# Kernel optimization log

Hardware: AMD Instinct MI355X
Metric: run time of the kernel (lower is better)

## Reference

```python
import jax, jax.numpy as jnp
import numpy as np

T, HID, HQ, HKV, D = 2048, 4096, 32, 8, 128
ROPE_BASE = 10000.0


def setup_inputs() -> dict:
    key = jax.random.key(0)
    ks = jax.random.split(key, 5)
    scale = 0.02
    hidden_states = jax.random.normal(ks[0], (T, HID), dtype=jnp.float32)
    position_ids = jnp.arange(T, dtype=jnp.int32)
    # HF-style rotary tables: freqs duplicated along last dim -> [T, D]
    inv_freq = 1.0 / (ROPE_BASE ** (jnp.arange(0, D, 2, dtype=jnp.float32) / D))
    ang = position_ids.astype(jnp.float32)[:, None] * inv_freq[None, :]  # [T, D/2]
    emb = jnp.concatenate([ang, ang], axis=-1)  # [T, D]
    cos, sin = jnp.cos(emb), jnp.sin(emb)
    Wq = jax.random.normal(ks[1], (HID, HQ * D), dtype=jnp.float32) * scale
    Wk = jax.random.normal(ks[2], (HID, HKV * D), dtype=jnp.float32) * scale
    Wv = jax.random.normal(ks[3], (HID, HKV * D), dtype=jnp.float32) * scale
    Wo = jax.random.normal(ks[4], (HQ * D, HID), dtype=jnp.float32) * scale
    return {"hidden_states": hidden_states, "position_ids": position_ids,
            "cos": cos, "sin": sin, "Wq": Wq, "Wk": Wk, "Wv": Wv, "Wo": Wo}


def _rotate_half(x):
    x1, x2 = jnp.split(x, 2, axis=-1)
    return jnp.concatenate([-x2, x1], axis=-1)


def reference(hidden_states, position_ids, cos, sin, Wq, Wk, Wv, Wo):
    t = hidden_states.shape[0]
    scaling = D ** -0.5
    # QKV projections (attention_bias=False)
    q = (hidden_states @ Wq).reshape(t, HQ, D)   # [T, Hq, D]
    k = (hidden_states @ Wk).reshape(t, HKV, D)  # [T, Hkv, D]
    v = (hidden_states @ Wv).reshape(t, HKV, D)
    # RoPE: cos/sin [T, D] broadcast over heads
    c, s = cos[:, None, :], sin[:, None, :]
    q = q * c + _rotate_half(q) * s
    k = k * c + _rotate_half(k) * s
    # GQA: expand KV heads to query heads
    groups = HQ // HKV
    k = jnp.repeat(k, groups, axis=1)  # [T, Hq, D]
    v = jnp.repeat(v, groups, axis=1)
    # Causal attention
    scores = jnp.einsum('thd,shd->hts', q, k) * scaling  # [Hq, T, T]
    causal = jnp.tril(jnp.ones((t, t), dtype=bool))
    scores = jnp.where(causal[None], scores, jnp.finfo(scores.dtype).min)
    probs = jax.nn.softmax(scores, axis=-1)
    attn = jnp.einsum('hts,shd->thd', probs, v).reshape(t, HQ * D)
    return attn @ Wo
```

## Files before the change

kernel.cpp:

```cpp
#include <hip/hip_runtime.h>
#include <hip/hip_bf16.h>
#include <cstdint>
#include <cstddef>

#define T_DIM   2048
#define HID     4096
#define HQ      32
#define HKV     8
#define D_HEAD  128
#define QKV_N   6144
#define KOFF    4096
#define VOFF    5120

typedef __attribute__((ext_vector_type(8))) short short8;
typedef __attribute__((ext_vector_type(4))) float floatx4;

__device__ __forceinline__ ushort f2bf(float f) {
    union { float f; uint u; } v; v.f = f;
    uint r = v.u + 0x7fffu + ((v.u >> 16) & 1u);
    return (ushort)(r >> 16);
}
__device__ __forceinline__ float bf2f(ushort h) {
    union { uint u; float f; } v; v.u = ((uint)h) << 16; return v.f;
}
__device__ __forceinline__ short8 ld8(const ushort* p) {
    uint2 a = *(const uint2*)p, b = *(const uint2*)(p + 4);
    union { uint u[4]; short8 s; } x;
    x.u[0] = a.x; x.u[1] = a.y; x.u[2] = b.x; x.u[3] = b.y;
    return x.s;
}
__device__ __forceinline__ void gld_lds16(const ushort* g, ushort* l) {
    __builtin_amdgcn_global_load_lds(
        (__attribute__((address_space(1))) void*)(g),
        (__attribute__((address_space(3))) void*)(l), 16, 0, 0);
}

__global__ void cast_f32_bf16(const float* __restrict__ in, ushort* __restrict__ out, int n) {
    int i = (blockIdx.x * blockDim.x + threadIdx.x) * 4;
    if (i < n) {
        float4 v = *(const float4*)(in + i);
        ushort4 o;
        o.x = f2bf(v.x); o.y = f2bf(v.y); o.z = f2bf(v.z); o.w = f2bf(v.w);
        *(ushort4*)(out + i) = o;
    }
}

__global__ __launch_bounds__(256) void transpose_cast(const float* __restrict__ W,
                                                      ushort* __restrict__ Wt, int K, int N) {
    __shared__ ushort tile[64][66];
    int n0 = blockIdx.x * 64, k0 = blockIdx.y * 64;
    int tx = threadIdx.x & 15, ty = threadIdx.x >> 4;
#pragma unroll
    for (int i = 0; i < 4; i++) {
        int r = ty + i * 16;
        float4 v = *(const float4*)&W[(size_t)(k0 + r) * N + n0 + tx * 4];
        tile[tx * 4 + 0][r] = f2bf(v.x);
        tile[tx * 4 + 1][r] = f2bf(v.y);
        tile[tx * 4 + 2][r] = f2bf(v.z);
        tile[tx * 4 + 3][r] = f2bf(v.w);
    }
    __syncthreads();
#pragma unroll
    for (int i = 0; i < 4; i++) {
        int nr = ty + i * 16;
        ushort4 o = *(const ushort4*)&tile[nr][tx * 4];
        *(ushort4*)&Wt[(size_t)(n0 + nr) * K + k0 + tx * 4] = o;
    }
}

__global__ void transpose_v(const ushort* __restrict__ qkv, ushort* __restrict__ VtG) {
    __shared__ ushort tile[32][33];
    int t0 = blockIdx.x * 32, d0 = blockIdx.y * 32, kvh = blockIdx.z;
    int tx = threadIdx.x & 31, ty = threadIdx.x >> 5;
#pragma unroll
    for (int i = 0; i < 4; i++) {
        int t = t0 + ty + i * 8;
        tile[ty + i * 8][tx] = qkv[(size_t)t * QKV_N + VOFF + kvh * D_HEAD + d0 + tx];
    }
    __syncthreads();
#pragma unroll
    for (int i = 0; i < 4; i++) {
        int d = d0 + ty + i * 8;
        VtG[((size_t)kvh * D_HEAD + d) * T_DIM + t0 + tx] = tile[tx][ty + i * 8];
    }
}

template <typename OutT>
__global__ __launch_bounds__(256) void gemm_bt(const ushort* __restrict__ A,
                                               const ushort* __restrict__ Bt,
                                               OutT* __restrict__ C,
                                               int K, int lda, int ldb, int ldc) {
    __shared__ ushort As[2][128 * 32];
    __shared__ ushort Bs[2][128 * 32];
    int tid = threadIdx.x;
    int w = tid >> 6, lane = tid & 63, quad = lane >> 4, l15 = lane & 15;
    int wr = (w >> 1) * 64, wc = (w & 1) * 64;
    int m0 = blockIdx.x * 128, n0 = blockIdx.y * 128;

    floatx4 acc[4][4];
    floatx4 z = {0.f, 0.f, 0.f, 0.f};
#pragma unroll
    for (int i = 0; i < 4; i++)
#pragma unroll
        for (int j = 0; j < 4; j++) acc[i][j] = z;

    int arow = tid >> 2, ac = (tid & 3) * 8;
    const ushort* gA0 = A + (size_t)(m0 + arow) * lda + ac;
    const ushort* gA1 = A + (size_t)(m0 + arow + 64) * lda + ac;
    const ushort* gB0 = Bt + (size_t)(n0 + arow) * ldb + ac;
    const ushort* gB1 = Bt + (size_t)(n0 + arow + 64) * ldb + ac;

    gld_lds16(gA0, &As[0][tid * 8]);
    gld_lds16(gA1, &As[0][64 * 32 + tid * 8]);
    gld_lds16(gB0, &Bs[0][tid * 8]);
    gld_lds16(gB1, &Bs[0][64 * 32 + tid * 8]);
    gA0 += 32; gA1 += 32; gB0 += 32; gB1 += 32;

    int cur = 0;
    for (int k0 = 0; k0 < K; k0 += 32, cur ^= 1) {
        __syncthreads();
        if (k0 + 32 < K) {
            gld_lds16(gA0, &As[cur ^ 1][tid * 8]);
            gld_lds16(gA1, &As[cur ^ 1][64 * 32 + tid * 8]);
            gld_lds16(gB0, &Bs[cur ^ 1][tid * 8]);
            gld_lds16(gB1, &Bs[cur ^ 1][64 * 32 + tid * 8]);
            gA0 += 32; gA1 += 32; gB0 += 32; gB1 += 32;
        }

        short8 af[4];
#pragma unroll
        for (int i = 0; i < 4; i++)
            af[i] = *(const short8*)&As[cur][(wr + i * 16 + l15) * 32 + quad * 8];
#pragma unroll
        for (int j = 0; j < 4; j++) {
            short8 bf = *(const short8*)&Bs[cur][(wc + j * 16 + l15) * 32 + quad * 8];
#pragma unroll
            for (int i = 0; i < 4; i++)
                acc[i][j] = __builtin_amdgcn_mfma_f32_16x16x32_bf16(af[i], bf, acc[i][j], 0, 0, 0);
        }
    }

#pragma unroll
    for (int i = 0; i < 4; i++) {
        int row0 = m0 + wr + i * 16 + quad * 4;
#pragma unroll
        for (int j = 0; j < 4; j++) {
            int col = n0 + wc + j * 16 + l15;
#pragma unroll
            for (int r = 0; r < 4; r++) {
                float v = acc[i][j][r];
                if constexpr (sizeof(OutT) == 2)
                    C[(size_t)(row0 + r) * ldc + col] = (OutT)f2bf(v);
                else
                    C[(size_t)(row0 + r) * ldc + col] = v;
            }
        }
    }
}

__global__ void rope_kernel(ushort* __restrict__ qkv, const float* __restrict__ cosb,
                            const float* __restrict__ sinb) {
    int t = blockIdx.x;
    ushort* row = qkv + (size_t)t * QKV_N;
    const float* cr = cosb + (size_t)t * D_HEAD;
    const float* sr = sinb + (size_t)t * D_HEAD;
    for (int c = threadIdx.x; c < 2560; c += 256) {
        int slice = c >> 6, d = c & 63;
        int col = slice * 128 + d;
        float x0 = bf2f(row[col]), x1 = bf2f(row[col + 64]);
        float cs = cr[d], sn = sr[d];
        row[col] = f2bf(x0 * cs - x1 * sn);
        row[col + 64] = f2bf(x1 * cs + x0 * sn);
    }
}

#define PS_STRIDE 68

__global__ __launch_bounds__(256, 2) void attn_kernel(const ushort* __restrict__ qkv,
                                                      const ushort* __restrict__ VtG,
                                                      ushort* __restrict__ attn) {
    __shared__ ushort Ks[64 * 128];
    __shared__ ushort Vt[128 * 64];
    __shared__ ushort Ps[128 * PS_STRIDE];

    int qt = (gridDim.x - 1) - blockIdx.x;
    int h = blockIdx.y;
    int q0 = qt * 128;
    int kbmax = 2 * qt + 1;
    int tid = threadIdx.x, w = tid >> 6, lane = tid & 63, quad = lane >> 4, l15 = lane & 15;
    int kvh = h >> 2;

    const ushort* kbase = qkv + (size_t)KOFF + (size_t)kvh * D_HEAD;
    const ushort* vbase = VtG + (size_t)kvh * D_HEAD * T_DIM;

    const ushort* ksrc[4];
    const ushort* vsrc[4];
#pragma unroll
    for (int i = 0; i < 4; i++) {
        int cid = i * 256 + tid;
        int kr = cid >> 4, kp = cid & 15, kc = kp ^ (kr & 15);
        ksrc[i] = kbase + (size_t)kr * QKV_N + kc * 8;
        int vr = cid >> 3, vp = cid & 7, vc = vp ^ (vr & 7);
        vsrc[i] = vbase + (size_t)vr * T_DIM + vc * 8;
    }

#pragma unroll
    for (int i = 0; i < 4; i++) {
        gld_lds16(ksrc[i], &Ks[(i * 256 + tid) * 8]);
        ksrc[i] += (size_t)64 * QKV_N;
    }

    short8 qf[2][4];
#pragma unroll
    for (int s = 0; s < 2; s++) {
        const ushort* qrow = qkv + (size_t)(q0 + s * 64 + w * 16 + l15) * QKV_N + h * D_HEAD + quad * 8;
#pragma unroll
        for (int ks = 0; ks < 4; ks++)
            qf[s][ks] = *(const short8*)(qrow + ks * 32);
    }

    floatx4 o[2][8];
    floatx4 z = {0.f, 0.f, 0.f, 0.f};
#pragma unroll
    for (int s = 0; s < 2; s++)
#pragma unroll
        for (int j = 0; j < 8; j++) o[s][j] = z;
    float lsum[2][4] = {{0.f, 0.f, 0.f, 0.f}, {0.f, 0.f, 0.f, 0.f}};

    const float scale_l2e = 0.08838834764831845f * 1.4426950408889634f;
    const float BOUND = 24.0f;

    __syncthreads();

    for (int kb = 0; kb <= kbmax; kb++) {
        bool act0 = (kb <= 2 * qt);

#pragma unroll
        for (int i = 0; i < 4; i++) {
            gld_lds16(vsrc[i], &Vt[(i * 256 + tid) * 8]);
            vsrc[i] += 64;
        }

        floatx4 sc[2][4];
#pragma unroll
        for (int s = 0; s < 2; s++)
#pragma unroll
            for (int jt = 0; jt < 4; jt++) sc[s][jt] = z;
#pragma unroll
        for (int ks = 0; ks < 4; ks++) {
#pragma unroll
            for (int jt = 0; jt < 4; jt++) {
                short8 kf = ld8(&Ks[(jt * 16 + l15) * 128 + (((ks * 4 + quad) ^ l15) * 8)]);
                if (act0)
                    sc[0][jt] = __builtin_amdgcn_mfma_f32_16x16x32_bf16(qf[0][ks], kf, sc[0][jt], 0, 0, 0);
                sc[1][jt] = __builtin_amdgcn_mfma_f32_16x16x32_bf16(qf[1][ks], kf, sc[1][jt], 0, 0, 0);
            }
        }

#pragma unroll
        for (int s = 0; s < 2; s++) {
            if (s == 0 && !act0) continue;
            bool diag = (kb == 2 * qt + s);
#pragma unroll
            for (int r = 0; r < 4; r++) {
                int rloc = w * 16 + quad * 4 + r;
#pragma unroll
                for (int jt = 0; jt < 4; jt++) {
                    float v = fmaf(sc[s][jt][r], scale_l2e, -BOUND);
                    if (diag && (jt * 16 + l15 > rloc)) v = -1e30f;
                    float p = exp2f(v);
                    lsum[s][r] += p;
                    Ps[(s * 64 + rloc) * PS_STRIDE + jt * 16 + l15] = f2bf(p);
                }
            }
        }

        __syncthreads();

        if (kb < kbmax) {
#pragma unroll
            for (int i = 0; i < 4; i++) {
                gld_lds16(ksrc[i], &Ks[(i * 256 + tid) * 8]);
                ksrc[i] += (size_t)64 * QKV_N;
            }
        }

#pragma unroll
        for (int ks2 = 0; ks2 < 2; ks2++) {
            short8 pf0 = ld8(&Ps[(w * 16 + l15) * PS_STRIDE + ks2 * 32 + quad * 8]);
            short8 pf1 = ld8(&Ps[(64 + w * 16 + l15) * PS_STRIDE + ks2 * 32 + quad * 8]);
#pragma unroll
            for (int jt = 0; jt < 8; jt++) {
                short8 vf = ld8(&Vt[(jt * 16 + l15) * 64 + (((ks2 * 4 + quad) ^ (l15 & 7)) * 8)]);
                if (act0)
                    o[0][jt] = __builtin_amdgcn_mfma_f32_16x16x32_bf16(pf0, vf, o[0][jt], 0, 0, 0);
                o[1][jt] = __builtin_amdgcn_mfma_f32_16x16x32_bf16(pf1, vf, o[1][jt], 0, 0, 0);
            }
        }

        __syncthreads();
    }

#pragma unroll
    for (int s = 0; s < 2; s++) {
#pragma unroll
        for (int r = 0; r < 4; r++) {
            float l = lsum[s][r];
#pragma unroll
            for (int mk = 1; mk <= 8; mk <<= 1) l += __shfl_xor(l, mk);
            float inv = 1.f / l;
            int trow = q0 + s * 64 + w * 16 + quad * 4 + r;
            ushort* orow = attn + (size_t)trow * (HQ * D_HEAD) + h * D_HEAD;
#pragma unroll
            for (int jt = 0; jt < 8; jt++)
                orow[jt * 16 + l15] = f2bf(o[s][jt][r] * inv);
        }
    }
}

extern "C" void kernel_launch(void* const* d_in, const int* in_sizes, int n_in,
                              void* d_out, int out_size, void* d_ws, size_t ws_size,
                              hipStream_t stream) {
    const float* hidden = (const float*)d_in[0];
    const float* cosb = (const float*)d_in[2];
    const float* sinb = (const float*)d_in[3];
    const float* Wq = (const float*)d_in[4];
    const float* Wk = (const float*)d_in[5];
    const float* Wv = (const float*)d_in[6];
    const float* Wo = (const float*)d_in[7];
    float* out = (float*)d_out;

    char* ws = (char*)d_ws;
    ushort* hiddenB = (ushort*)(ws);
    ushort* WqkvT   = (ushort*)(ws + (size_t)(16u << 20));
    ushort* WoT     = (ushort*)(ws + (size_t)(64u << 20));
    ushort* qkv     = (ushort*)(ws + (size_t)(96u << 20));
    ushort* attnO   = (ushort*)(ws + (size_t)(120u << 20));
    ushort* VtG     = (ushort*)(ws + (size_t)(136u << 20));

    cast_f32_bf16<<<8192, 256, 0, stream>>>(hidden, hiddenB, T_DIM * HID);
    transpose_cast<<<dim3(64, 64), 256, 0, stream>>>(Wq, WqkvT, HID, 4096);
    transpose_cast<<<dim3(16, 64), 256, 0, stream>>>(Wk, WqkvT + (size_t)4096 * HID, HID, 1024);
    transpose_cast<<<dim3(16, 64), 256, 0, stream>>>(Wv, WqkvT + (size_t)5120 * HID, HID, 1024);
    transpose_cast<<<dim3(64, 64), 256, 0, stream>>>(Wo, WoT, HID, 4096);

    gemm_bt<ushort><<<dim3(16, 48), 256, 0, stream>>>(hiddenB, WqkvT, qkv,
                                                      HID, HID, HID, QKV_N);
    rope_kernel<<<T_DIM, 256, 0, stream>>>(qkv, cosb, sinb);
    transpose_v<<<dim3(64, 4, 8), 256, 0, stream>>>(qkv, VtG);
    attn_kernel<<<dim3(T_DIM / 128, HQ), 256, 0, stream>>>(qkv, VtG, attnO);
    gemm_bt<float><<<dim3(16, 32), 256, 0, stream>>>(attnO, WoT, out,
                                                     HID, HID, HID, HID);
}
```

Measured before the change: 542.4 us.

## Replace GEMM with 256x256-tile, 4-stage pipelined, swizzled-LDS 8-wave kernel

Swaps the 128x128 double-buffered GEMM for a 256x256 tile kernel with 512 threads, a 4-deep LDS ring buffer with prefetch three steps ahead, XOR-swizzled LDS layout to avoid bank conflicts, and explicit waitcnt/barrier/setprio scheduling to overlap loads with MFMA. The goal is more data reuse per tile and better hiding of global-load latency in both projection GEMMs. In exchange, LDS use is large (128KB) and the grid is small (192 and 128 blocks), which may underfill the CUs. The manual vmcnt bookkeeping also risks subtle hazards.

```diff
diff --git a/kernel.cpp b/kernel.cpp
--- a/kernel.cpp
+++ b/kernel.cpp
@@ -86,68 +86,107 @@
 }
 
 template <typename OutT>
-__global__ __launch_bounds__(256) void gemm_bt(const ushort* __restrict__ A,
-                                               const ushort* __restrict__ Bt,
-                                               OutT* __restrict__ C,
-                                               int K, int lda, int ldb, int ldc) {
-    __shared__ ushort As[2][128 * 32];
-    __shared__ ushort Bs[2][128 * 32];
+__global__ __launch_bounds__(512, 2) void gemm_bt2(const ushort* __restrict__ A,
+                                                   const ushort* __restrict__ Bt,
+                                                   OutT* __restrict__ C,
+                                                   int K, int lda, int ldb, int ldc) {
+    __shared__ ushort As[4][256 * 32];
+    __shared__ ushort Bs[4][256 * 32];
     int tid = threadIdx.x;
-    int w = tid >> 6, lane = tid & 63, quad = lane >> 4, l15 = lane & 15;
-    int wr = (w >> 1) * 64, wc = (w & 1) * 64;
-    int m0 = blockIdx.x * 128, n0 = blockIdx.y * 128;
-
-    floatx4 acc[4][4];
+    int wid = tid >> 6, lane = tid & 63, quad = lane >> 4, l15 = lane & 15;
+    int wr = wid >> 2, wc = wid & 3;
+    int m0 = blockIdx.x * 256, n0 = blockIdx.y * 256;
+
+    floatx4 acc[8][4];
     floatx4 z = {0.f, 0.f, 0.f, 0.f};
 #pragma unroll
-    for (int i = 0; i < 4; i++)
+    for (int i = 0; i < 8; i++)
 #pragma unroll
         for (int j = 0; j < 4; j++) acc[i][j] = z;
 
-    int arow = tid >> 2, ac = (tid & 3) * 8;
-    const ushort* gA0 = A + (size_t)(m0 + arow) * lda + ac;
-    const ushort* gA1 = A + (size_t)(m0 + arow + 64) * lda + ac;
-    const ushort* gB0 = Bt + (size_t)(n0 + arow) * ldb + ac;
-    const ushort* gB1 = Bt + (size_t)(n0 + arow + 64) * ldb + ac;
-
-    gld_lds16(gA0, &As[0][tid * 8]);
-    gld_lds16(gA1, &As[0][64 * 32 + tid * 8]);
-    gld_lds16(gB0, &Bs[0][tid * 8]);
-    gld_lds16(gB1, &Bs[0][64 * 32 + tid * 8]);
-    gA0 += 32; gA1 += 32; gB0 += 32; gB1 += 32;
-
-    int cur = 0;
-    for (int k0 = 0; k0 < K; k0 += 32, cur ^= 1) {
-        __syncthreads();
-        if (k0 + 32 < K) {
-            gld_lds16(gA0, &As[cur ^ 1][tid * 8]);
-            gld_lds16(gA1, &As[cur ^ 1][64 * 32 + tid * 8]);
-            gld_lds16(gB0, &Bs[cur ^ 1][tid * 8]);
-            gld_lds16(gB1, &Bs[cur ^ 1][64 * 32 + tid * 8]);
-            gA0 += 32; gA1 += 32; gB0 += 32; gB1 += 32;
-        }
-
-        short8 af[4];
-#pragma unroll
-        for (int i = 0; i < 4; i++)
-            af[i] = *(const short8*)&As[cur][(wr + i * 16 + l15) * 32 + quad * 8];
-#pragma unroll
-        for (int j = 0; j < 4; j++) {
-            short8 bf = *(const short8*)&Bs[cur][(wc + j * 16 + l15) * 32 + quad * 8];
-#pragma unroll
-            for (int i = 0; i < 4; i++)
-                acc[i][j] = __builtin_amdgcn_mfma_f32_16x16x32_bf16(af[i], bf, acc[i][j], 0, 0, 0);
-        }
-    }
-
-#pragma unroll
-    for (int i = 0; i < 4; i++) {
-        int row0 = m0 + wr + i * 16 + quad * 4;
-#pragma unroll
-        for (int j = 0; j < 4; j++) {
-            int col = n0 + wc + j * 16 + l15;
-#pragma unroll
-            for (int r = 0; r < 4; r++) {
+    int NK = K >> 5;
+
+    int r_st = tid >> 2;
+    int c_st = (tid & 3) ^ ((tid >> 3) & 3);
+    const ushort* gA0 = A  + (size_t)(m0 + r_st)       * lda + c_st * 8;
+    const ushort* gA1 = A  + (size_t)(m0 + 128 + r_st) * lda + c_st * 8;
+    const ushort* gB0 = Bt + (size_t)(n0 + r_st)       * ldb + c_st * 8;
+    const ushort* gB1 = Bt + (size_t)(n0 + 128 + r_st) * ldb + c_st * 8;
+
+    for (int s = 0; s < 3; ++s) {
+        gld_lds16(gA0 + s * 32, &As[s][tid * 8]);
+        gld_lds16(gA1 + s * 32, &As[s][4096 + tid * 8]);
+        gld_lds16(gB0 + s * 32, &Bs[s][tid * 8]);
+        gld_lds16(gB1 + s * 32, &Bs[s][4096 + tid * 8]);
+    }
+    asm volatile("s_waitcnt vmcnt(8)" ::: "memory");
+    __builtin_amdgcn_s_barrier();
+
+    short8 af[4];
+    short8 bf[4];
+    for (int s = 0; s < NK; ++s) {
+        const ushort* sA = &As[s & 3][0];
+        const ushort* sB = &Bs[s & 3][0];
+
+#pragma unroll
+        for (int n = 0; n < 4; ++n) {
+            int row = wc * 64 + n * 16 + l15;
+            bf[n] = *(const short8*)&sB[row * 32 + ((quad ^ ((row >> 1) & 3)) * 8)];
+        }
+#pragma unroll
+        for (int mi = 0; mi < 4; ++mi) {
+            int row = wr * 128 + mi * 16 + l15;
+            af[mi] = *(const short8*)&sA[row * 32 + ((quad ^ ((row >> 1) & 3)) * 8)];
+        }
+        if (s + 3 < NK) {
+            gld_lds16(gA0 + (s + 3) * 32, &As[(s + 3) & 3][tid * 8]);
+            gld_lds16(gA1 + (s + 3) * 32, &As[(s + 3) & 3][4096 + tid * 8]);
+        }
+        __builtin_amdgcn_sched_barrier(0);
+        __builtin_amdgcn_s_barrier();
+        __builtin_amdgcn_s_setprio(1);
+#pragma unroll
+        for (int n = 0; n < 4; ++n)
+#pragma unroll
+            for (int mi = 0; mi < 4; ++mi)
+                acc[mi][n] = __builtin_amdgcn_mfma_f32_16x16x32_bf16(af[mi], bf[n], acc[mi][n], 0, 0, 0);
+        __builtin_amdgcn_s_setprio(0);
+        __builtin_amdgcn_sched_barrier(0);
+        __builtin_amdgcn_s_barrier();
+
+#pragma unroll
+        for (int mi = 0; mi < 4; ++mi) {
+            int row = wr * 128 + 64 + mi * 16 + l15;
+            af[mi] = *(const short8*)&sA[row * 32 + ((quad ^ ((row >> 1) & 3)) * 8)];
+        }
+        if (s + 3 < NK) {
+            gld_lds16(gB0 + (s + 3) * 32, &Bs[(s + 3) & 3][tid * 8]);
+            gld_lds16(gB1 + (s + 3) * 32, &Bs[(s + 3) & 3][4096 + tid * 8]);
+        }
+        __builtin_amdgcn_sched_barrier(0);
+        __builtin_amdgcn_s_barrier();
+        __builtin_amdgcn_s_setprio(1);
+#pragma unroll
+        for (int n = 0; n < 4; ++n)
+#pragma unroll
+            for (int mi = 0; mi < 4; ++mi)
+                acc[4 + mi][n] = __builtin_amdgcn_mfma_f32_16x16x32_bf16(af[mi], bf[n], acc[4 + mi][n], 0, 0, 0);
+        __builtin_amdgcn_s_setprio(0);
+        if (s < NK - 3)       asm volatile("s_waitcnt vmcnt(8)" ::: "memory");
+        else if (s == NK - 3) asm volatile("s_waitcnt vmcnt(4)" ::: "memory");
+        else if (s == NK - 2) asm volatile("s_waitcnt vmcnt(0)" ::: "memory");
+        __builtin_amdgcn_sched_barrier(0);
+        __builtin_amdgcn_s_barrier();
+    }
+
+#pragma unroll
+    for (int i = 0; i < 8; ++i) {
+        int row0 = m0 + wr * 128 + i * 16 + quad * 4;
+#pragma unroll
+        for (int j = 0; j < 4; ++j) {
+            int col = n0 + wc * 64 + j * 16 + l15;
+#pragma unroll
+            for (int r = 0; r < 4; ++r) {
                 float v = acc[i][j][r];
                 if constexpr (sizeof(OutT) == 2)
                     C[(size_t)(row0 + r) * ldc + col] = (OutT)f2bf(v);
@@ -344,11 +383,11 @@
     transpose_cast<<<dim3(16, 64), 256, 0, stream>>>(Wv, WqkvT + (size_t)5120 * HID, HID, 1024);
     transpose_cast<<<dim3(64, 64), 256, 0, stream>>>(Wo, WoT, HID, 4096);
 
-    gemm_bt<ushort><<<dim3(16, 48), 256, 0, stream>>>(hiddenB, WqkvT, qkv,
+    gemm_bt2<ushort><<<dim3(8, 24), 512, 0, stream>>>(hiddenB, WqkvT, qkv,
                                                       HID, HID, HID, QKV_N);
     rope_kernel<<<T_DIM, 256, 0, stream>>>(qkv, cosb, sinb);
     transpose_v<<<dim3(64, 4, 8), 256, 0, stream>>>(qkv, VtG);
     attn_kernel<<<dim3(T_DIM / 128, HQ), 256, 0, stream>>>(qkv, VtG, attnO);
-    gemm_bt<float><<<dim3(16, 32), 256, 0, stream>>>(attnO, WoT, out,
+    gemm_bt2<float><<<dim3(8, 16), 512, 0, stream>>>(attnO, WoT, out,
                                                      HID, HID, HID, HID);
 }
```

New measurement: 594.3 us. +9.6%, slower.

## Add 256x256-tile 8-wave GEMM with interleaved prefetch for QKV projection

Applied to the files above, without the earlier changes.

Adds a new GEMM kernel with 256x256 output tiles, 512 threads, XOR-swizzled LDS, and a double-buffered pipeline. Global-to-LDS loads for the next K slice are split into four chunks and interleaved between MFMA phases, with explicit waitcnt, barriers and priority hints. It is used only for the QKV projection. The aim is more data reuse per block and better overlap of memory with compute. The trade-off is a larger register and LDS footprint and only 192 blocks, which may underfill the GPU's compute units.

```diff
diff --git a/kernel.cpp b/kernel.cpp
--- a/kernel.cpp
+++ b/kernel.cpp
@@ -82,6 +82,190 @@
     for (int i = 0; i < 4; i++) {
         int d = d0 + ty + i * 8;
         VtG[((size_t)kvh * D_HEAD + d) * T_DIM + t0 + tx] = tile[tx][ty + i * 8];
+    }
+}
+
+template <typename OutT>
+__global__ __launch_bounds__(512, 2) void gemm256(const ushort* __restrict__ A,
+                                                  const ushort* __restrict__ Bt,
+                                                  OutT* __restrict__ C,
+                                                  int K, int lda, int ldb, int ldc) {
+    __shared__ ushort As[2][16384];
+    __shared__ ushort Bs[2][16384];
+    int tid = threadIdx.x;
+    int wid = tid >> 6, lane = tid & 63, quad = lane >> 4, l15 = lane & 15;
+    int wr = wid >> 2, wc = wid & 3;
+    int bh = wc >> 1, br = (wc & 1) * 64;
+    int m0 = blockIdx.x * 256, n0 = blockIdx.y * 256;
+    int sw = (l15 & 7);
+
+    floatx4 acc[8][4];
+    floatx4 z = {0.f, 0.f, 0.f, 0.f};
+#pragma unroll
+    for (int i = 0; i < 8; i++)
+#pragma unroll
+        for (int j = 0; j < 4; j++) acc[i][j] = z;
+
+    int NT = K >> 6;
+
+    int r8 = tid >> 3;
+    int csw = (tid & 7) ^ (r8 & 7);
+    const ushort* sA = A  + (size_t)(m0 + r8) * lda + csw * 8;
+    const ushort* sB = Bt + (size_t)(n0 + r8) * ldb + csw * 8;
+
+    gld_lds16(sA,                          &As[0][tid * 8]);
+    gld_lds16(sA + (size_t)128 * lda,      &As[0][8192 + tid * 8]);
+    gld_lds16(sB,                          &Bs[0][tid * 8]);
+    gld_lds16(sB + (size_t)128 * ldb,      &Bs[0][8192 + tid * 8]);
+    gld_lds16(sB + (size_t)64 * ldb,       &Bs[0][4096 + tid * 8]);
+    gld_lds16(sB + (size_t)192 * ldb,      &Bs[0][12288 + tid * 8]);
+    gld_lds16(sA + (size_t)64 * lda,       &As[0][4096 + tid * 8]);
+    gld_lds16(sA + (size_t)192 * lda,      &As[0][12288 + tid * 8]);
+    asm volatile("s_waitcnt vmcnt(2)" ::: "memory");
+    __builtin_amdgcn_sched_barrier(0);
+    __builtin_amdgcn_s_barrier();
+
+    short8 bfr[4][2];
+    short8 af[2][2];
+
+    for (int t = 0; t < NT; ++t) {
+        int slot = t & 1, ns = slot ^ 1;
+        const ushort* tA = &As[slot][wr * 8192];
+        const ushort* tB = &Bs[slot][bh * 8192];
+        size_t ko = (size_t)(t + 1) * 64;
+        bool pf = (t + 1 < NT);
+
+#pragma unroll
+        for (int nf = 0; nf < 4; ++nf)
+#pragma unroll
+            for (int kh = 0; kh < 2; ++kh)
+                bfr[nf][kh] = *(const short8*)&tB[(br + nf * 16 + l15) * 64 +
+                                                  (((quad + kh * 4) ^ sw) * 8)];
+#pragma unroll
+        for (int mi = 0; mi < 2; ++mi)
+#pragma unroll
+            for (int kh = 0; kh < 2; ++kh)
+                af[mi][kh] = *(const short8*)&tA[(mi * 16 + l15) * 64 +
+                                                 (((quad + kh * 4) ^ sw) * 8)];
+        if (pf) {
+            gld_lds16(sA + ko,                     &As[ns][tid * 8]);
+            gld_lds16(sA + (size_t)128 * lda + ko, &As[ns][8192 + tid * 8]);
+        }
+        __builtin_amdgcn_sched_barrier(0);
+        __builtin_amdgcn_s_barrier();
+        asm volatile("s_waitcnt lgkmcnt(0)" ::: "memory");
+        __builtin_amdgcn_sched_barrier(0);
+        __builtin_amdgcn_s_setprio(1);
+#pragma unroll
+        for (int nf = 0; nf < 4; ++nf)
+#pragma unroll
+            for (int mi = 0; mi < 2; ++mi)
+#pragma unroll
+                for (int kh = 0; kh < 2; ++kh)
+                    acc[mi][nf] = __builtin_amdgcn_mfma_f32_16x16x32_bf16(af[mi][kh], bfr[nf][kh], acc[mi][nf], 0, 0, 0);
+        __builtin_amdgcn_s_setprio(0);
+        __builtin_amdgcn_sched_barrier(0);
+        __builtin_amdgcn_s_barrier();
+
+#pragma unroll
+        for (int mi = 0; mi < 2; ++mi)
+#pragma unroll
+            for (int kh = 0; kh < 2; ++kh)
+                af[mi][kh] = *(const short8*)&tA[(32 + mi * 16 + l15) * 64 +
+                                                 (((quad + kh * 4) ^ sw) * 8)];
+        if (pf) {
+            gld_lds16(sB + ko,                     &Bs[ns][tid * 8]);
+            gld_lds16(sB + (size_t)128 * ldb + ko, &Bs[ns][8192 + tid * 8]);
+        }
+        __builtin_amdgcn_sched_barrier(0);
+        __builtin_amdgcn_s_barrier();
+        asm volatile("s_waitcnt lgkmcnt(0)" ::: "memory");
+        __builtin_amdgcn_sched_barrier(0);
+        __builtin_amdgcn_s_setprio(1);
+#pragma unroll
+        for (int nf = 0; nf < 4; ++nf)
+#pragma unroll
+            for (int mi = 0; mi < 2; ++mi)
+#pragma unroll
+                for (int kh = 0; kh < 2; ++kh)
+                    acc[2 + mi][nf] = __builtin_amdgcn_mfma_f32_16x16x32_bf16(af[mi][kh], bfr[nf][kh], acc[2 + mi][nf], 0, 0, 0);
+        __builtin_amdgcn_s_setprio(0);
+        __builtin_amdgcn_sched_barrier(0);
+        if (pf) asm volatile("s_waitcnt vmcnt(4)" ::: "memory");
+        else    asm volatile("s_waitcnt vmcnt(0)" ::: "memory");
+        __builtin_amdgcn_sched_barrier(0);
+        __builtin_amdgcn_s_barrier();
+
+#pragma unroll
+        for (int mi = 0; mi < 2; ++mi)
+#pragma unroll
+            for (int kh = 0; kh < 2; ++kh)
+                af[mi][kh] = *(const short8*)&tA[(64 + mi * 16 + l15) * 64 +
+                                                 (((quad + kh * 4) ^ sw) * 8)];
+        if (pf) {
+            gld_lds16(sB + (size_t)64 * ldb + ko,  &Bs[ns][4096 + tid * 8]);
+            gld_lds16(sB + (size_t)192 * ldb + ko, &Bs[ns][12288 + tid * 8]);
+        }
+        __builtin_amdgcn_sched_barrier(0);
+        __builtin_amdgcn_s_barrier();
+        asm volatile("s_waitcnt lgkmcnt(0)" ::: "memory");
+        __builtin_amdgcn_sched_barrier(0);
+        __builtin_amdgcn_s_setprio(1);
+#pragma unroll
+        for (int nf = 0; nf < 4; ++nf)
+#pragma unroll
+            for (int mi = 0; mi < 2; ++mi)
+#pragma unroll
+                for (int kh = 0; kh < 2; ++kh)
+                    acc[4 + mi][nf] = __builtin_amdgcn_mfma_f32_16x16x32_bf16(af[mi][kh], bfr[nf][kh], acc[4 + mi][nf], 0, 0, 0);
+        __builtin_amdgcn_s_setprio(0);
+        __builtin_amdgcn_sched_barrier(0);
+        __builtin_amdgcn_s_barrier();
+
+#pragma unroll
+        for (int mi = 0; mi < 2; ++mi)
+#pragma unroll
+            for (int kh = 0; kh < 2; ++kh)
+                af[mi][kh] = *(const short8*)&tA[(96 + mi * 16 + l15) * 64 +
+                                                 (((quad + kh * 4) ^ sw) * 8)];
+        if (pf) {
+            gld_lds16(sA + (size_t)64 * lda + ko,  &As[ns][4096 + tid * 8]);
+            gld_lds16(sA + (size_t)192 * lda + ko, &As[ns][12288 + tid * 8]);
+        }
+        __builtin_amdgcn_sched_barrier(0);
+        __builtin_amdgcn_s_barrier();
+        asm volatile("s_waitcnt lgkmcnt(0)" ::: "memory");
+        __builtin_amdgcn_sched_barrier(0);
+        __builtin_amdgcn_s_setprio(1);
+#pragma unroll
+        for (int nf = 0; nf < 4; ++nf)
+#pragma unroll
+            for (int mi = 0; mi < 2; ++mi)
+#pragma unroll
+                for (int kh = 0; kh < 2; ++kh)
+                    acc[6 + mi][nf] = __builtin_amdgcn_mfma_f32_16x16x32_bf16(af[mi][kh], bfr[nf][kh], acc[6 + mi][nf], 0, 0, 0);
+        __builtin_amdgcn_s_setprio(0);
+        __builtin_amdgcn_sched_barrier(0);
+        if (pf) asm volatile("s_waitcnt vmcnt(2)" ::: "memory");
+        __builtin_amdgcn_sched_barrier(0);
+        __builtin_amdgcn_s_barrier();
+    }
+
+#pragma unroll
+    for (int i = 0; i < 8; ++i) {
+        int row0 = m0 + wr * 128 + i * 16 + quad * 4;
+#pragma unroll
+        for (int j = 0; j < 4; ++j) {
+            int col = n0 + wc * 64 + j * 16 + l15;
+#pragma unroll
+            for (int r = 0; r < 4; ++r) {
+                float v = acc[i][j][r];
+                if constexpr (sizeof(OutT) == 2)
+                    C[(size_t)(row0 + r) * ldc + col] = (OutT)f2bf(v);
+                else
+                    C[(size_t)(row0 + r) * ldc + col] = v;
+            }
+        }
     }
 }
 
@@ -344,8 +528,8 @@
     transpose_cast<<<dim3(16, 64), 256, 0, stream>>>(Wv, WqkvT + (size_t)5120 * HID, HID, 1024);
     transpose_cast<<<dim3(64, 64), 256, 0, stream>>>(Wo, WoT, HID, 4096);
 
-    gemm_bt<ushort><<<dim3(16, 48), 256, 0, stream>>>(hiddenB, WqkvT, qkv,
-                                                      HID, HID, HID, QKV_N);
+    gemm256<ushort><<<dim3(8, 24), 512, 0, stream>>>(hiddenB, WqkvT, qkv,
+                                                     HID, HID, HID, QKV_N);
     rope_kernel<<<T_DIM, 256, 0, stream>>>(qkv, cosb, sinb);
     transpose_v<<<dim3(64, 4, 8), 256, 0, stream>>>(qkv, VtG);
     attn_kernel<<<dim3(T_DIM / 128, HQ), 256, 0, stream>>>(qkv, VtG, attnO);
```

Measured after the change: 569.8 us. 1.05x slower.
